# Kernel optimization log

Measured on AMD Instinct MI355X. Metric: run time of the kernel, lower is better.

Reference implementation:

```python
import jax, jax.numpy as jnp
import numpy as np

N = 100_000   # total vertices
E = 1_600_000 # total directed edges
B = 64        # graphs in batch
HID = 128
DM = 256
EPS = 1e-5


def _linear_init(k, fan_in, fan_out):
    lim = 1.0 / np.sqrt(fan_in)
    kw, kb = jax.random.split(k)
    W = jax.random.uniform(kw, (fan_in, fan_out), minval=-lim, maxval=lim, dtype=jnp.float32)
    b = jax.random.uniform(kb, (fan_out,), minval=-lim, maxval=lim, dtype=jnp.float32)
    return W, b


def setup_inputs() -> dict:
    key = jax.random.key(0)
    ks = jax.random.split(key, 8)
    W_in, b_in = _linear_init(ks[0], 3, HID)
    W1, b1 = _linear_init(ks[1], HID, HID)
    W2, b2 = _linear_init(ks[2], HID, HID)
    W3, b3 = _linear_init(ks[3], HID, HID)
    W_out, b_out = _linear_init(ks[4], HID, DM)
    vertices = jax.random.normal(ks[5], (N, 3), dtype=jnp.float32)
    edge_index = jax.random.randint(ks[6], (2, E), 0, N)
    batch = jnp.sort(jax.random.randint(ks[7], (N,), 0, B))
    gamma = jnp.ones((DM,), jnp.float32)
    beta = jnp.zeros((DM,), jnp.float32)
    return dict(vertices=vertices, edge_index=edge_index, batch=batch,
                W_in=W_in, b_in=b_in, W1=W1, b1=b1, W2=W2, b2=b2, W3=W3, b3=b3,
                W_out=W_out, b_out=b_out, gamma=gamma, beta=beta)


def _gcn_conv(x, W, b, src, dst):
    # PyG GCNConv: add self-loops, sym-normalize by deg^{-1/2}, aggregate at dst.
    h = x @ W  # [N, HID]
    deg = jnp.zeros((x.shape[0],), x.dtype).at[dst].add(1.0) + 1.0  # +1 self-loop
    dinv = jax.lax.rsqrt(deg)
    msg = h[src] * (dinv[src] * dinv[dst])[:, None]       # [E, HID] gather+scale
    agg = jnp.zeros_like(h).at[dst].add(msg)               # scatter-add
    agg = agg + h * (dinv * dinv)[:, None]                 # self-loop contribution
    return agg + b


def reference(vertices, edge_index, batch, W_in, b_in, W1, b1, W2, b2, W3, b3, W_out, b_out, gamma, beta):
    src, dst = edge_index[0], edge_index[1]
    x = vertices @ W_in + b_in
    for W, b in ((W1, b1), (W2, b2), (W3, b3)):
        x = jax.nn.relu(_gcn_conv(x, W, b, src, dst))
    # global_mean_pool over batch segments
    summ = jax.ops.segment_sum(x, batch, num_segments=B)
    cnt = jax.ops.segment_sum(jnp.ones((x.shape[0], 1), x.dtype), batch, num_segments=B)
    pooled = summ / jnp.maximum(cnt, 1.0)
    y = pooled @ W_out + b_out
    mu = jnp.mean(y, axis=-1, keepdims=True)
    var = jnp.var(y, axis=-1, keepdims=True)
    return (y - mu) * jax.lax.rsqrt(var + EPS) * gamma + beta
```

## Files before the change

kernel.cpp:

```cpp
#include <hip/hip_runtime.h>

constexpr int NV = 100000;
constexpr int NE = 1600000;
constexpr int NB = 64;
constexpr int HD = 128;
constexpr int DM = 256;
#define EPSLN 1e-5f

constexpr int DPB   = 512;
constexpr int NBUCK = (NV + DPB - 1) / DPB;
constexpr int BCAP  = 16384;
constexpr int EPB2  = 2048;
constexpr int NEB2  = (NE + EPB2 - 1) / EPB2;
constexpr int H1B   = 1024;
constexpr int WTB   = 128;
constexpr int LCAP  = 12288;

typedef short bf16x8 __attribute__((ext_vector_type(8)));
typedef float f32x4 __attribute__((ext_vector_type(4)));

__device__ inline unsigned short f2b(float f) {
    union { float f; unsigned u; } x; x.f = f;
    unsigned r = x.u + 0x7FFF + ((x.u >> 16) & 1);
    return (unsigned short)(r >> 16);
}
__device__ inline float b2f(unsigned short h) {
    union { unsigned u; float f; } x; x.u = (unsigned)h << 16;
    return x.f;
}

__global__ __launch_bounds__(256) void k_init(const float* __restrict__ verts,
                                              const float* __restrict__ Win,
                                              const float* __restrict__ bin,
                                              const float* __restrict__ W1,
                                              const float* __restrict__ W2,
                                              const float* __restrict__ W3,
                                              const int* __restrict__ ei,
                                              int* __restrict__ bcursor,
                                              int* __restrict__ ebuf,
                                              unsigned short* __restrict__ Hb,
                                              unsigned short* __restrict__ Wt) {
    int t = threadIdx.x;
    int bid = blockIdx.x;
    if (bid < NEB2) {
        __shared__ int h[NBUCK];
        __shared__ int lbase[NBUCK];
        for (int i = t; i < NBUCK; i += 256) h[i] = 0;
        __syncthreads();
        int base = bid * EPB2;
        int s[8], d[8], rk[8];
        #pragma unroll
        for (int j = 0; j < 8; ++j) {
            int idx = base + j * 256 + t;
            if (idx < NE) {
                s[j] = ei[idx];
                d[j] = ei[NE + idx];
                rk[j] = atomicAdd(&h[d[j] >> 9], 1);
            } else d[j] = -1;
        }
        __syncthreads();
        for (int i = t; i < NBUCK; i += 256) {
            int c = h[i];
            if (c) lbase[i] = atomicAdd(&bcursor[i], c);
        }
        __syncthreads();
        #pragma unroll
        for (int j = 0; j < 8; ++j)
            if (d[j] >= 0) {
                int b = d[j] >> 9;
                ebuf[(b << 14) + lbase[b] + rk[j]] = (s[j] << 9) | (d[j] & 511);
            }
        return;
    }
    if (bid < NEB2 + H1B) {
        __shared__ float Wc[3 * HD];
        __shared__ float bc[HD];
        if (t < HD) {
            float w0 = 0.f, w1 = 0.f, w2 = 0.f, bv = 0.f;
            for (int k = 0; k < HD; ++k) {
                float w = W1[k * HD + t];
                w0 = fmaf(Win[k], w, w0);
                w1 = fmaf(Win[128 + k], w, w1);
                w2 = fmaf(Win[256 + k], w, w2);
                bv = fmaf(bin[k], w, bv);
            }
            Wc[t] = w0; Wc[128 + t] = w1; Wc[256 + t] = w2; bc[t] = bv;
        }
        __syncthreads();
        for (int idx = (bid - NEB2) * 256 + t; idx < NV * HD; idx += H1B * 256) {
            int v = idx >> 7, c = idx & 127;
            float a = verts[v * 3 + 0], b = verts[v * 3 + 1], d = verts[v * 3 + 2];
            Hb[idx] = f2b(bc[c] + a * Wc[c] + b * Wc[128 + c] + d * Wc[256 + c]);
        }
        return;
    }
    int idx = (bid - NEB2 - H1B) * 256 + t;
    if (idx < 2 * HD * HD) {
        int l = idx >> 14, r = idx & 16383;
        const float* W = (l == 0) ? W2 : W3;
        int n = r >> 7, k = r & 127;
        Wt[(l << 14) + n * HD + k] = f2b(W[k * HD + n]);
    }
}

__global__ __launch_bounds__(512) void k_bcsr(const int* __restrict__ ebuf,
                                              const int* __restrict__ bcursor,
                                              int* __restrict__ degi,
                                              float* __restrict__ dinv,
                                              int* __restrict__ rowstart,
                                              int* __restrict__ csr) {
    __shared__ int els[LCAP];
    __shared__ int h[DPB];
    __shared__ int sdata[DPB];
    int b = blockIdx.x, t = threadIdx.x, d0 = b * DPB;
    if (t < DPB) h[t] = 0;
    __syncthreads();
    int e0 = b << 14;
    int n = bcursor[b];
    for (int i = t; i < n; i += 512) {
        int p = ebuf[e0 + i];
        if (i < LCAP) els[i] = p;
        atomicAdd(&h[p & 511], 1);
    }
    __syncthreads();
    int a = h[t];
    sdata[t] = a;
    __syncthreads();
    for (int off = 1; off < 512; off <<= 1) {
        int v = sdata[t];
        int add = (t >= off) ? sdata[t - off] : 0;
        __syncthreads();
        sdata[t] = v + add;
        __syncthreads();
    }
    int excl = (t == 0) ? 0 : sdata[t - 1];
    int v0 = d0 + t;
    if (v0 < NV) {
        rowstart[v0] = e0 + excl;
        degi[v0] = a;
        dinv[v0] = rsqrtf((float)a + 1.0f);
    }
    h[t] = e0 + excl;
    __syncthreads();
    for (int i = t; i < n; i += 512) {
        int p = (i < LCAP) ? els[i] : ebuf[e0 + i];
        int slot = atomicAdd(&h[p & 511], 1);
        csr[slot] = p >> 9;
    }
}

__global__ __launch_bounds__(256) void k_gemm_mfma(const unsigned short* __restrict__ Xb,
                                                   const unsigned short* __restrict__ Wt,
                                                   unsigned short* __restrict__ Hb) {
    __shared__ __align__(16) unsigned short Ws[128 * 132];
    __shared__ __align__(16) unsigned short hs[4][16][136];
    int t = threadIdx.x;
    {
        int row = t >> 1;
        int half = (t & 1) << 6;
        const unsigned short* src = Wt + row * HD + half;
        unsigned short* dst = &Ws[row * 132 + half];
        #pragma unroll
        for (int i = 0; i < 8; ++i)
            *(bf16x8*)(dst + i * 8) = *(const bf16x8*)(src + i * 8);
    }
    int wave = t >> 6;
    int lane = t & 63;
    int r = lane & 15;
    int g = lane >> 4;
    int row0 = blockIdx.x * 64 + wave * 16;
    int arow = row0 + r;
    bool valid = arow < NV;

    bf16x8 afrag[4];
    const unsigned short* xp = Xb + (size_t)arow * HD + g * 8;
    #pragma unroll
    for (int ks = 0; ks < 4; ++ks) {
        if (valid) afrag[ks] = *(const bf16x8*)(xp + ks * 32);
        else       afrag[ks] = bf16x8{0, 0, 0, 0, 0, 0, 0, 0};
    }
    __syncthreads();

    #pragma unroll
    for (int nt = 0; nt < 8; ++nt) {
        f32x4 acc = {0.f, 0.f, 0.f, 0.f};
        #pragma unroll
        for (int ks = 0; ks < 4; ++ks) {
            bf16x8 bfrag = *(const bf16x8*)&Ws[(nt * 16 + r) * 132 + g * 8 + ks * 32];
            acc = __builtin_amdgcn_mfma_f32_16x16x32_bf16(afrag[ks], bfrag, acc, 0, 0, 0);
        }
        #pragma unroll
        for (int j = 0; j < 4; ++j)
            hs[wave][g * 4 + j][nt * 16 + r] = f2b(acc[j]);
    }
    int row = lane >> 2;
    int grow = row0 + row;
    #pragma unroll
    for (int k = 0; k < 4; ++k) {
        int c = (lane & 3) + k * 4;
        bf16x8 val = *(const bf16x8*)&hs[wave][row][c * 8];
        if (grow < NV)
            *(bf16x8*)(Hb + (size_t)grow * HD + c * 8) = val;
    }
}

__global__ __launch_bounds__(256) void k_agg(const unsigned short* __restrict__ H,
                                             const float* __restrict__ dinv,
                                             const int* __restrict__ rowstart,
                                             const int* __restrict__ degi,
                                             const int* __restrict__ csr_src,
                                             const float* __restrict__ bias,
                                             unsigned short* __restrict__ Xo) {
    int gtid = blockIdx.x * 256 + threadIdx.x;
    int v = gtid >> 6;
    if (v >= NV) return;
    int lane = threadIdx.x & 63;
    int q = lane >> 4;
    int l4 = lane & 15;
    float di = dinv[v];
    int rs = rowstart[v], len = degi[v];
    float a[8];
    if (q == 0) {
        float sc = di * di;
        bf16x8 hv = *(const bf16x8*)(H + (size_t)v * HD + l4 * 8);
        #pragma unroll
        for (int jj = 0; jj < 8; ++jj) a[jj] = b2f((unsigned short)hv[jj]) * sc;
    } else {
        #pragma unroll
        for (int jj = 0; jj < 8; ++jj) a[jj] = 0.f;
    }
    int cnt = (len - q + 3) >> 2;
    int idx = rs + q;
    int j = 0;
    for (; j + 1 < cnt; j += 2) {
        int s0 = csr_src[idx], s1 = csr_src[idx + 4];
        idx += 8;
        float w0 = dinv[s0] * di, w1 = dinv[s1] * di;
        bf16x8 h0 = *(const bf16x8*)(H + (size_t)s0 * HD + l4 * 8);
        bf16x8 h1 = *(const bf16x8*)(H + (size_t)s1 * HD + l4 * 8);
        #pragma unroll
        for (int jj = 0; jj < 8; ++jj) {
            a[jj] = fmaf(b2f((unsigned short)h0[jj]), w0, a[jj]);
            a[jj] = fmaf(b2f((unsigned short)h1[jj]), w1, a[jj]);
        }
    }
    if (j < cnt) {
        int s0 = csr_src[idx];
        float w0 = dinv[s0] * di;
        bf16x8 h0 = *(const bf16x8*)(H + (size_t)s0 * HD + l4 * 8);
        #pragma unroll
        for (int jj = 0; jj < 8; ++jj)
            a[jj] = fmaf(b2f((unsigned short)h0[jj]), w0, a[jj]);
    }
    #pragma unroll
    for (int jj = 0; jj < 8; ++jj) {
        a[jj] += __shfl_xor(a[jj], 16);
        a[jj] += __shfl_xor(a[jj], 32);
    }
    if (q == 0) {
        bf16x8 ov;
        #pragma unroll
        for (int jj = 0; jj < 8; ++jj)
            ov[jj] = (short)f2b(fmaxf(a[jj] + bias[l4 * 8 + jj], 0.f));
        *(bf16x8*)(Xo + (size_t)v * HD + l4 * 8) = ov;
    }
}

__global__ __launch_bounds__(256) void k_pool(const unsigned short* __restrict__ X,
                                              const int* __restrict__ batch,
                                              float* __restrict__ pool,
                                              int* __restrict__ cnt) {
    constexpr int CHUNK = (NV + 2047) / 2048;
    __shared__ float lp[2][HD];
    __shared__ int binfo[2];
    int t = threadIdx.x;
    int v0 = blockIdx.x * CHUNK;
    if (v0 >= NV) return;
    int vend = min(v0 + CHUNK, NV);
    if (t < 2 * HD) ((float*)lp)[t] = 0.f;
    if (t == 0) { binfo[0] = batch[v0]; binfo[1] = batch[vend - 1]; }
    __syncthreads();
    int b0 = binfo[0], b1 = binfo[1];
    int cg = t & 15;
    int ro = t >> 4;
    if (b1 - b0 <= 1) {
        float a0[8] = {}, a1[8] = {};
        for (int v = v0 + ro; v < vend; v += 16) {
            bf16x8 x = *(const bf16x8*)(X + (size_t)v * HD + cg * 8);
            if (batch[v] == b0) {
                #pragma unroll
                for (int jj = 0; jj < 8; ++jj) a0[jj] += b2f((unsigned short)x[jj]);
            } else {
                #pragma unroll
                for (int jj = 0; jj < 8; ++jj) a1[jj] += b2f((unsigned short)x[jj]);
            }
        }
        #pragma unroll
        for (int jj = 0; jj < 8; ++jj) {
            atomicAdd(&lp[0][cg * 8 + jj], a0[jj]);
            if (b1 != b0) atomicAdd(&lp[1][cg * 8 + jj], a1[jj]);
        }
        __syncthreads();
        int slot = t >> 7, col = t & 127;
        if (slot == 0 || b1 != b0)
            atomicAdd(&pool[(slot ? b1 : b0) * HD + col], lp[slot][col]);
    } else {
        float a[8] = {};
        int cur = -1;
        for (int v = v0 + ro; v < vend; v += 16) {
            int bb = batch[v];
            if (bb != cur) {
                if (cur >= 0) {
                    #pragma unroll
                    for (int jj = 0; jj < 8; ++jj) {
                        atomicAdd(&pool[cur * HD + cg * 8 + jj], a[jj]);
                        a[jj] = 0.f;
                    }
                }
                cur = bb;
            }
            bf16x8 x = *(const bf16x8*)(X + (size_t)v * HD + cg * 8);
            #pragma unroll
            for (int jj = 0; jj < 8; ++jj) a[jj] += b2f((unsigned short)x[jj]);
        }
        if (cur >= 0) {
            #pragma unroll
            for (int jj = 0; jj < 8; ++jj)
                atomicAdd(&pool[cur * HD + cg * 8 + jj], a[jj]);
        }
    }
    if (t == 0) {
        int prev = batch[v0], c0 = 0;
        for (int v = v0; v < vend; ++v) {
            int bb = batch[v];
            if (bb != prev) { atomicAdd(&cnt[prev], c0); prev = bb; c0 = 0; }
            ++c0;
        }
        atomicAdd(&cnt[prev], c0);
    }
}

__global__ __launch_bounds__(256) void k_out(const float* __restrict__ pool,
                                             const int* __restrict__ cnt,
                                             const float* __restrict__ Wout,
                                             const float* __restrict__ bout,
                                             const float* __restrict__ gamma,
                                             const float* __restrict__ beta,
                                             float* __restrict__ out) {
    __shared__ float ps[HD];
    __shared__ float red[DM];
    int g = blockIdx.x, t = threadIdx.x;
    if (t < HD) {
        float cn = fmaxf((float)cnt[g], 1.0f);
        ps[t] = pool[g * HD + t] / cn;
    }
    __syncthreads();
    float acc = bout[t];
    #pragma unroll 8
    for (int k = 0; k < HD; ++k) acc = fmaf(ps[k], Wout[k * DM + t], acc);
    red[t] = acc; __syncthreads();
    for (int s2 = 128; s2 > 0; s2 >>= 1) {
        if (t < s2) red[t] += red[t + s2];
        __syncthreads();
    }
    float mu = red[0] * (1.0f / DM);
    __syncthreads();
    float d = acc - mu;
    red[t] = d * d; __syncthreads();
    for (int s2 = 128; s2 > 0; s2 >>= 1) {
        if (t < s2) red[t] += red[t + s2];
        __syncthreads();
    }
    float var = red[0] * (1.0f / DM);
    out[g * DM + t] = d * rsqrtf(var + EPSLN) * gamma[t] + beta[t];
}

extern "C" void kernel_launch(void* const* d_in, const int* in_sizes, int n_in,
                              void* d_out, int out_size, void* d_ws, size_t ws_size,
                              hipStream_t stream) {
    const float* verts = (const float*)d_in[0];
    const int*   ei    = (const int*)d_in[1];
    const int*   batch = (const int*)d_in[2];
    const float* Win   = (const float*)d_in[3];
    const float* bin   = (const float*)d_in[4];
    const float* W1    = (const float*)d_in[5];
    const float* b1    = (const float*)d_in[6];
    const float* W2    = (const float*)d_in[7];
    const float* b2    = (const float*)d_in[8];
    const float* W3    = (const float*)d_in[9];
    const float* b3    = (const float*)d_in[10];
    const float* Wout  = (const float*)d_in[11];
    const float* bout  = (const float*)d_in[12];
    const float* gamma = (const float*)d_in[13];
    const float* beta  = (const float*)d_in[14];
    float* out = (float*)d_out;

    char* wp = (char*)d_ws;
    auto alloc = [&](size_t bytes) -> char* {
        char* p = wp;
        wp += (bytes + 255) & ~(size_t)255;
        return p;
    };
    unsigned short* bufA = (unsigned short*)alloc((size_t)NV * HD * 2);
    unsigned short* bufB = (unsigned short*)alloc((size_t)NV * HD * 2);
    unsigned short* Wt   = (unsigned short*)alloc((size_t)2 * HD * HD * 2);
    int*   degi     = (int*)alloc((size_t)NV * 4);
    float* dinv     = (float*)alloc((size_t)NV * 4);
    int*   rowstart = (int*)alloc((size_t)NV * 4);
    int*   csr      = (int*)alloc((size_t)NBUCK * BCAP * 4);
    int*   ebuf     = (int*)alloc((size_t)NBUCK * BCAP * 4);
    char*  zblock   = alloc(1024 + (size_t)NB * HD * 4 + 1024);
    int*   bcursor  = (int*)zblock;
    float* pool     = (float*)(zblock + 1024);
    int*   cnt      = (int*)(zblock + 1024 + (size_t)NB * HD * 4);

    hipMemsetAsync(zblock, 0, 1024 + (size_t)NB * HD * 4 + 1024, stream);

    k_init<<<NEB2 + H1B + WTB, 256, 0, stream>>>(verts, Win, bin, W1, W2, W3,
                                                 ei, bcursor, ebuf, bufA, Wt);
    k_bcsr<<<NBUCK, 512, 0, stream>>>(ebuf, bcursor, degi, dinv, rowstart, csr);

    int aggrid = (int)(((size_t)NV * 64 + 255) / 256);
    k_agg<<<aggrid, 256, 0, stream>>>(bufA, dinv, rowstart, degi, csr, b1, bufB);
    k_gemm_mfma<<<(NV + 63) / 64, 256, 0, stream>>>(bufB, Wt, bufA);
    k_agg<<<aggrid, 256, 0, stream>>>(bufA, dinv, rowstart, degi, csr, b2, bufB);
    k_gemm_mfma<<<(NV + 63) / 64, 256, 0, stream>>>(bufB, Wt + (size_t)HD * HD, bufA);
    k_agg<<<aggrid, 256, 0, stream>>>(bufA, dinv, rowstart, degi, csr, b3, bufB);

    k_pool<<<2048, 256, 0, stream>>>(bufB, batch, pool, cnt);
    k_out<<<NB, 256, 0, stream>>>(pool, cnt, Wout, bout, gamma, beta, out);
}
```

Baseline: 339.5 us.

## Halve CSR bucket size and compute graph counts from sorted batch boundaries

Buckets now cover 256 destination vertices instead of 512. This gives 391 smaller buckets, so each k_bcsr block runs 256 threads and keeps the whole bucket in shared memory. The per-vertex cnt loop, run serially by one thread in k_pool, is replaced by extra k_init blocks that record each graph's start and end from the sorted batch array; k_out divides by gend-gstart. The trade-offs are a larger shared-memory histogram in k_init (391 bins) and more bucket bookkeeping. BCAP=8192 at about 4096 expected edges per bucket leaves less headroom than before.

After: 340.3 us. About the same (+0.2%).

```diff
diff --git a/kernel.cpp b/kernel.cpp
--- a/kernel.cpp
+++ b/kernel.cpp
@@ -7,14 +7,15 @@
 constexpr int DM = 256;
 #define EPSLN 1e-5f
 
-constexpr int DPB   = 512;
+constexpr int DPB   = 256;
 constexpr int NBUCK = (NV + DPB - 1) / DPB;
-constexpr int BCAP  = 16384;
+constexpr int BCAP  = 8192;
+constexpr int BSH   = 13;
 constexpr int EPB2  = 2048;
 constexpr int NEB2  = (NE + EPB2 - 1) / EPB2;
 constexpr int H1B   = 1024;
 constexpr int WTB   = 128;
-constexpr int LCAP  = 12288;
+constexpr int BDB   = (NV + 255) / 256;
 
 typedef short bf16x8 __attribute__((ext_vector_type(8)));
 typedef float f32x4 __attribute__((ext_vector_type(4)));
@@ -36,10 +37,13 @@
                                               const float* __restrict__ W2,
                                               const float* __restrict__ W3,
                                               const int* __restrict__ ei,
+                                              const int* __restrict__ batch,
                                               int* __restrict__ bcursor,
                                               int* __restrict__ ebuf,
                                               unsigned short* __restrict__ Hb,
-                                              unsigned short* __restrict__ Wt) {
+                                              unsigned short* __restrict__ Wt,
+                                              int* __restrict__ gstart,
+                                              int* __restrict__ gend) {
     int t = threadIdx.x;
     int bid = blockIdx.x;
     if (bid < NEB2) {
@@ -55,7 +59,7 @@
             if (idx < NE) {
                 s[j] = ei[idx];
                 d[j] = ei[NE + idx];
-                rk[j] = atomicAdd(&h[d[j] >> 9], 1);
+                rk[j] = atomicAdd(&h[d[j] >> 8], 1);
             } else d[j] = -1;
         }
         __syncthreads();
@@ -67,8 +71,8 @@
         #pragma unroll
         for (int j = 0; j < 8; ++j)
             if (d[j] >= 0) {
-                int b = d[j] >> 9;
-                ebuf[(b << 14) + lbase[b] + rk[j]] = (s[j] << 9) | (d[j] & 511);
+                int b = d[j] >> 8;
+                ebuf[(b << BSH) + lbase[b] + rk[j]] = (s[j] << 8) | (d[j] & 255);
             }
         return;
     }
@@ -94,39 +98,49 @@
         }
         return;
     }
-    int idx = (bid - NEB2 - H1B) * 256 + t;
-    if (idx < 2 * HD * HD) {
-        int l = idx >> 14, r = idx & 16383;
-        const float* W = (l == 0) ? W2 : W3;
-        int n = r >> 7, k = r & 127;
-        Wt[(l << 14) + n * HD + k] = f2b(W[k * HD + n]);
-    }
-}
-
-__global__ __launch_bounds__(512) void k_bcsr(const int* __restrict__ ebuf,
+    if (bid < NEB2 + H1B + WTB) {
+        int idx = (bid - NEB2 - H1B) * 256 + t;
+        if (idx < 2 * HD * HD) {
+            int l = idx >> 14, r = idx & 16383;
+            const float* W = (l == 0) ? W2 : W3;
+            int n = r >> 7, k = r & 127;
+            Wt[(l << 14) + n * HD + k] = f2b(W[k * HD + n]);
+        }
+        return;
+    }
+    int i = (bid - NEB2 - H1B - WTB) * 256 + t;
+    if (i < NV) {
+        int b = batch[i];
+        if (i == 0 || batch[i - 1] != b) gstart[b] = i;
+        int bn = (i + 1 < NV) ? batch[i + 1] : -1;
+        if (bn != b) gend[b] = i + 1;
+    }
+}
+
+__global__ __launch_bounds__(256) void k_bcsr(const int* __restrict__ ebuf,
                                               const int* __restrict__ bcursor,
                                               int* __restrict__ degi,
                                               float* __restrict__ dinv,
                                               int* __restrict__ rowstart,
                                               int* __restrict__ csr) {
-    __shared__ int els[LCAP];
+    __shared__ int els[BCAP];
     __shared__ int h[DPB];
     __shared__ int sdata[DPB];
     int b = blockIdx.x, t = threadIdx.x, d0 = b * DPB;
-    if (t < DPB) h[t] = 0;
-    __syncthreads();
-    int e0 = b << 14;
+    h[t] = 0;
+    __syncthreads();
+    int e0 = b << BSH;
     int n = bcursor[b];
-    for (int i = t; i < n; i += 512) {
+    for (int i = t; i < n; i += 256) {
         int p = ebuf[e0 + i];
-        if (i < LCAP) els[i] = p;
-        atomicAdd(&h[p & 511], 1);
+        if (i < BCAP) els[i] = p;
+        atomicAdd(&h[p & 255], 1);
     }
     __syncthreads();
     int a = h[t];
     sdata[t] = a;
     __syncthreads();
-    for (int off = 1; off < 512; off <<= 1) {
+    for (int off = 1; off < 256; off <<= 1) {
         int v = sdata[t];
         int add = (t >= off) ? sdata[t - off] : 0;
         __syncthreads();
@@ -142,10 +156,10 @@
     }
     h[t] = e0 + excl;
     __syncthreads();
-    for (int i = t; i < n; i += 512) {
-        int p = (i < LCAP) ? els[i] : ebuf[e0 + i];
-        int slot = atomicAdd(&h[p & 511], 1);
-        csr[slot] = p >> 9;
+    for (int i = t; i < n; i += 256) {
+        int p = (i < BCAP) ? els[i] : ebuf[e0 + i];
+        int slot = atomicAdd(&h[p & 255], 1);
+        csr[slot] = p >> 8;
     }
 }
 
@@ -268,8 +282,7 @@
 
 __global__ __launch_bounds__(256) void k_pool(const unsigned short* __restrict__ X,
                                               const int* __restrict__ batch,
-                                              float* __restrict__ pool,
-                                              int* __restrict__ cnt) {
+                                              float* __restrict__ pool) {
     constexpr int CHUNK = (NV + 2047) / 2048;
     __shared__ float lp[2][HD];
     __shared__ int binfo[2];
@@ -329,19 +342,11 @@
                 atomicAdd(&pool[cur * HD + cg * 8 + jj], a[jj]);
         }
     }
-    if (t == 0) {
-        int prev = batch[v0], c0 = 0;
-        for (int v = v0; v < vend; ++v) {
-            int bb = batch[v];
-            if (bb != prev) { atomicAdd(&cnt[prev], c0); prev = bb; c0 = 0; }
-            ++c0;
-        }
-        atomicAdd(&cnt[prev], c0);
-    }
 }
 
 __global__ __launch_bounds__(256) void k_out(const float* __restrict__ pool,
-                                             const int* __restrict__ cnt,
+                                             const int* __restrict__ gstart,
+                                             const int* __restrict__ gend,
                                              const float* __restrict__ Wout,
                                              const float* __restrict__ bout,
                                              const float* __restrict__ gamma,
@@ -351,7 +356,7 @@
     __shared__ float red[DM];
     int g = blockIdx.x, t = threadIdx.x;
     if (t < HD) {
-        float cn = fmaxf((float)cnt[g], 1.0f);
+        float cn = fmaxf((float)(gend[g] - gstart[g]), 1.0f);
         ps[t] = pool[g * HD + t] / cn;
     }
     __syncthreads();
@@ -409,16 +414,21 @@
     int*   rowstart = (int*)alloc((size_t)NV * 4);
     int*   csr      = (int*)alloc((size_t)NBUCK * BCAP * 4);
     int*   ebuf     = (int*)alloc((size_t)NBUCK * BCAP * 4);
-    char*  zblock   = alloc(1024 + (size_t)NB * HD * 4 + 1024);
+    size_t zb_cursor = ((size_t)NBUCK * 4 + 255) & ~(size_t)255;
+    size_t zb_pool   = (size_t)NB * HD * 4;
+    size_t zb_tot    = zb_cursor + zb_pool + 1024;
+    char*  zblock   = alloc(zb_tot);
     int*   bcursor  = (int*)zblock;
-    float* pool     = (float*)(zblock + 1024);
-    int*   cnt      = (int*)(zblock + 1024 + (size_t)NB * HD * 4);
-
-    hipMemsetAsync(zblock, 0, 1024 + (size_t)NB * HD * 4 + 1024, stream);
-
-    k_init<<<NEB2 + H1B + WTB, 256, 0, stream>>>(verts, Win, bin, W1, W2, W3,
-                                                 ei, bcursor, ebuf, bufA, Wt);
-    k_bcsr<<<NBUCK, 512, 0, stream>>>(ebuf, bcursor, degi, dinv, rowstart, csr);
+    float* pool     = (float*)(zblock + zb_cursor);
+    int*   gstart   = (int*)(zblock + zb_cursor + zb_pool);
+    int*   gend     = (int*)(zblock + zb_cursor + zb_pool + 512);
+
+    hipMemsetAsync(zblock, 0, zb_tot, stream);
+
+    k_init<<<NEB2 + H1B + WTB + BDB, 256, 0, stream>>>(verts, Win, bin, W1, W2, W3,
+                                                       ei, batch, bcursor, ebuf,
+                                                       bufA, Wt, gstart, gend);
+    k_bcsr<<<NBUCK, 256, 0, stream>>>(ebuf, bcursor, degi, dinv, rowstart, csr);
 
     int aggrid = (int)(((size_t)NV * 64 + 255) / 256);
     k_agg<<<aggrid, 256, 0, stream>>>(bufA, dinv, rowstart, degi, csr, b1, bufB);
@@ -427,6 +437,6 @@
     k_gemm_mfma<<<(NV + 63) / 64, 256, 0, stream>>>(bufB, Wt + (size_t)HD * HD, bufA);
     k_agg<<<aggrid, 256, 0, stream>>>(bufA, dinv, rowstart, degi, csr, b3, bufB);
 
-    k_pool<<<2048, 256, 0, stream>>>(bufB, batch, pool, cnt);
-    k_out<<<NB, 256, 0, stream>>>(pool, cnt, Wout, bout, gamma, beta, out);
-}
+    k_pool<<<2048, 256, 0, stream>>>(bufB, batch, pool);
+    k_out<<<NB, 256, 0, stream>>>(pool, gstart, gend, Wout, bout, gamma, beta, out);
+}
```
